# Kernel tuning notes

Hardware: AMD Instinct MI355X
Metric: run time of the kernel (lower is better)

## Reference

```python
import jax, jax.numpy as jnp
import numpy as np

SEQ, BATCH, EMBED = 1024, 2, 768
E = 16            # num_experts = m * N = 2 * 8
FFN_H = 1536      # expert_dim = ceil(3072 / 2)
K_SHARED = 1
K_ROUTE = 3       # (m * top_k) - k_shared = 4 - 1
LN_EPS = 1e-5
NEG_INF = -1e9


def setup_inputs() -> dict:
    key = jax.random.key(0)
    ks = jax.random.split(key, 4)
    x = jax.random.normal(ks[0], (SEQ, BATCH, EMBED), dtype=jnp.float32)
    gate_w = jax.random.normal(ks[1], (EMBED, E), dtype=jnp.float32) * 0.02
    gate_b = jnp.zeros((E,), jnp.float32)
    fc1_w = jax.random.normal(ks[2], (E, EMBED, FFN_H), dtype=jnp.float32) * 0.02
    fc1_b = jnp.zeros((E, FFN_H), jnp.float32)
    ln_w = jnp.ones((E, FFN_H), jnp.float32)
    ln_b = jnp.zeros((E, FFN_H), jnp.float32)
    fc2_w = jax.random.normal(ks[3], (E, FFN_H, EMBED), dtype=jnp.float32) * 0.02
    fc2_b = jnp.zeros((E, EMBED), jnp.float32)
    return {"x": x, "gate_w": gate_w, "gate_b": gate_b,
            "fc1_w": fc1_w, "fc1_b": fc1_b, "ln_w": ln_w, "ln_b": ln_b,
            "fc2_w": fc2_w, "fc2_b": fc2_b}


def reference(x, gate_w, gate_b, fc1_w, fc1_b, ln_w, ln_b, fc2_w, fc2_b):
    S, B, D = x.shape
    T = S * B
    xf = x.reshape(T, D)

    # --- gating: mask shared-expert logits, softmax, top-k over routed probs ---
    scores = xf @ gate_w + gate_b                      # [T, E]
    scores = scores.at[:, :K_SHARED].set(NEG_INF)
    probs = jax.nn.softmax(scores, axis=-1)
    topv, topi = jax.lax.top_k(probs, K_ROUTE)         # [T, K_ROUTE]

    # combine weights: gate prob for selected routed experts, 1.0 for shared experts
    combine = jnp.zeros((T, E), xf.dtype)
    combine = combine.at[jnp.arange(T)[:, None], topi].add(topv)
    combine = combine.at[:, :K_SHARED].add(1.0)        # shared expert(s), weight 1

    # --- per-expert FFN (dense over experts; combine zeros out unselected) ---
    h = jnp.einsum('td,edh->eth', xf, fc1_w) + fc1_b[:, None, :]   # [E, T, H]
    h = jax.nn.gelu(h, approximate=False)              # torch nn.GELU = exact erf
    mu = h.mean(-1, keepdims=True)
    var = h.var(-1, keepdims=True)
    h = (h - mu) * jax.lax.rsqrt(var + LN_EPS) * ln_w[:, None, :] + ln_b[:, None, :]
    y = jnp.einsum('eth,ehd->etd', h, fc2_w) + fc2_b[:, None, :]   # [E, T, D]

    # --- scatter-add combine (gate-weighted sum over experts) ---
    out = jnp.einsum('te,etd->td', combine, y)
    return out.reshape(S, B, D)
```

## Files before the change

kernel.cpp:

```cpp
#include <hip/hip_runtime.h>
#include <cmath>

#define T_TOK 2048
#define D_EMB 768
#define H_FFN 1536
#define NE    16
#define NPAIR (T_TOK * 4)

typedef __attribute__((ext_vector_type(8))) short          short8;
typedef __attribute__((ext_vector_type(8))) unsigned short ushort8;
typedef __attribute__((ext_vector_type(4))) unsigned short ushort4v;
typedef __attribute__((ext_vector_type(4))) float          floatx4;

__device__ __forceinline__ float bf2f(unsigned short u) {
  union { unsigned int i; float f; } v; v.i = ((unsigned int)u) << 16; return v.f;
}
__device__ __forceinline__ unsigned short f2bf(float f) {
  union { float f; unsigned int i; } v; v.f = f;
  unsigned int r = v.i + 0x7fffu + ((v.i >> 16) & 1u);
  return (unsigned short)(r >> 16);
}

__device__ __forceinline__ void gload16(const unsigned short* g, unsigned short* l) {
  __builtin_amdgcn_global_load_lds(
      (const __attribute__((address_space(1))) unsigned int*)g,
      (__attribute__((address_space(3))) unsigned int*)l,
      16, 0, 0);
}

__global__ __launch_bounds__(64) void sniff_kernel(
    const unsigned int* __restrict__ x, int* __restrict__ flag)
{
  int lane = threadIdx.x;
  int c = 0;
  for (int i = 0; i < 8; i++) {
    unsigned int w = x[i * 64 + lane];
    unsigned int e = (w >> 7) & 0xFFu;
    c += (e >= 100u && e <= 140u) ? 1 : 0;
  }
  for (int off = 32; off > 0; off >>= 1) c += __shfl_down(c, off);
  if (lane == 0) *flag = (c > 300) ? 1 : 0;
}

__global__ __launch_bounds__(256) void conv_kernel(
    const float* __restrict__ x, const float* __restrict__ fc1b,
    const float* __restrict__ lnw, const float* __restrict__ lnb,
    const float* __restrict__ fc2b,
    unsigned short* __restrict__ dx, unsigned short* __restrict__ dfc1b,
    unsigned short* __restrict__ dlnw, unsigned short* __restrict__ dlnb,
    unsigned short* __restrict__ dfc2b, const int* __restrict__ flag)
{
  if (*flag) return;
  int g = blockIdx.x * 256 + threadIdx.x;
#pragma unroll
  for (int i = 0; i < 3; i++) dx[g + i * 524288] = f2bf(x[g + i * 524288]);
  if (g < 24576) { dfc1b[g] = f2bf(fc1b[g]); dlnw[g] = f2bf(lnw[g]); dlnb[g] = f2bf(lnb[g]); }
  if (g < 12288) dfc2b[g] = f2bf(fc2b[g]);
}

template<int R, int C>
__global__ __launch_bounds__(256) void transpose_kernel(
    const unsigned short* __restrict__ srcB, const float* __restrict__ srcF,
    const int* __restrict__ flag, unsigned short* __restrict__ dst)
{
  __shared__ __align__(16) unsigned short tile[64][72];
  constexpr int RT = R / 64, CT = C / 64;
  int bx  = blockIdx.x;
  int e   = bx / (RT * CT);
  int rem = bx % (RT * CT);
  int rt  = rem / CT, ct = rem % CT;
  int tid = threadIdx.x;
  int r   = tid >> 2;
  int c   = (tid & 3) * 16;
  int xr  = (r & 7) * 8;
  size_t sbase = ((size_t)e * R + rt * 64 + r) * C + ct * 64 + c;
  if (*flag) {
    ushort8 v0 = *(const ushort8*)(srcB + sbase);
    ushort8 v1 = *(const ushort8*)(srcB + sbase + 8);
    *(ushort8*)&tile[r][(c) ^ xr]     = v0;
    *(ushort8*)&tile[r][(c + 8) ^ xr] = v1;
  } else {
    unsigned short tmp[16];
#pragma unroll
    for (int q = 0; q < 4; q++) {
      floatx4 f = *(const floatx4*)(srcF + sbase + q * 4);
#pragma unroll
      for (int j = 0; j < 4; j++) tmp[q * 4 + j] = f2bf(f[j]);
    }
    *(ushort8*)&tile[r][(c) ^ xr]     = *(ushort8*)&tmp[0];
    *(ushort8*)&tile[r][(c + 8) ^ xr] = *(ushort8*)&tmp[8];
  }
  __syncthreads();
  int n  = tid >> 2;
  int k  = (tid & 3) * 16;
  unsigned short outv[16];
#pragma unroll
  for (int j = 0; j < 16; j++) {
    int kr = k + j;
    outv[j] = tile[kr][n ^ ((kr & 7) * 8)];
  }
  size_t dbase = ((size_t)e * C + ct * 64 + n) * R + rt * 64 + k;
  *(ushort8*)(dst + dbase)     = *(ushort8*)&outv[0];
  *(ushort8*)(dst + dbase + 8) = *(ushort8*)&outv[8];
}

__global__ __launch_bounds__(64) void gate_kernel(
    const unsigned short* __restrict__ x16, const float* __restrict__ x32,
    const unsigned short* __restrict__ gw16, const float* __restrict__ gw32,
    const unsigned short* __restrict__ gb16, const float* __restrict__ gb32,
    const int* __restrict__ flag,
    int* __restrict__ psel, float* __restrict__ pw)
{
  int t = blockIdx.x;
  int lane = threadIdx.x;
  int isbf = *flag;
  float acc[NE];
#pragma unroll
  for (int e = 0; e < NE; e++) acc[e] = 0.f;
  if (isbf) {
#pragma unroll
    for (int i = 0; i < D_EMB / 64; i++) {
      int d = i * 64 + lane;
      float xv = bf2f(x16[(size_t)t * D_EMB + d]);
      ushort8 g0 = *(const ushort8*)(gw16 + d * NE);
      ushort8 g1 = *(const ushort8*)(gw16 + d * NE + 8);
#pragma unroll
      for (int e = 0; e < 8; e++) acc[e]     += xv * bf2f(g0[e]);
#pragma unroll
      for (int e = 0; e < 8; e++) acc[8 + e] += xv * bf2f(g1[e]);
    }
  } else {
#pragma unroll
    for (int i = 0; i < D_EMB / 64; i++) {
      int d = i * 64 + lane;
      float xv = x32[(size_t)t * D_EMB + d];
#pragma unroll
      for (int q = 0; q < 4; q++) {
        floatx4 g = *(const floatx4*)(gw32 + d * NE + q * 4);
#pragma unroll
        for (int j = 0; j < 4; j++) acc[q * 4 + j] += xv * g[j];
      }
    }
  }
  __shared__ __align__(16) float sacc[64][NE + 1];
#pragma unroll
  for (int e = 0; e < NE; e++) sacc[lane][e] = acc[e];
  __syncthreads();
  int e = lane & 15, q = lane >> 4;
  float s = 0.f;
#pragma unroll
  for (int i = 0; i < 16; i++) s += sacc[q * 16 + i][e];
  s += __shfl_xor(s, 16);
  s += __shfl_xor(s, 32);
  float sv = s + (isbf ? bf2f(gb16[e]) : gb32[e]);
  if (e == 0) sv = -1e9f;
  float m = sv;
#pragma unroll
  for (int off = 8; off > 0; off >>= 1) m = fmaxf(m, __shfl_xor(m, off));
  float pe = expf(sv - m);
  float den = pe;
#pragma unroll
  for (int off = 8; off > 0; off >>= 1) den += __shfl_xor(den, off);
  float pr = pe / den;
  float val = (e == 0) ? -1.f : pr;
  int sel0, sel1, sel2; float sw0, sw1, sw2;
#pragma unroll
  for (int k = 0; k < 3; k++) {
    float bv = val; int bi = e;
#pragma unroll
    for (int off = 8; off > 0; off >>= 1) {
      float ov = __shfl_xor(bv, off);
      int   oi = __shfl_xor(bi, off);
      if (ov > bv || (ov == bv && oi < bi)) { bv = ov; bi = oi; }
    }
    if (k == 0) { sel0 = bi; sw0 = bv; }
    else if (k == 1) { sel1 = bi; sw1 = bv; }
    else { sel2 = bi; sw2 = bv; }
    if (e == bi) val = -1.f;
  }
  if (lane == 0) {
    psel[t * 4] = 0;    pw[t * 4] = 1.0f;
    psel[t * 4 + 1] = sel0; pw[t * 4 + 1] = sw0;
    psel[t * 4 + 2] = sel1; pw[t * 4 + 2] = sw1;
    psel[t * 4 + 3] = sel2; pw[t * 4 + 3] = sw2;
  }
}

__global__ __launch_bounds__(256) void bucket_kernel(
    const int* __restrict__ psel, int* __restrict__ cnt, int* __restrict__ plist)
{
  int e = blockIdx.x;
  int tid = threadIdx.x;
  int wave = tid >> 6, lane = tid & 63;
  __shared__ int wsum[4];
  __shared__ int base;
  if (tid == 0) base = 0;
  __syncthreads();
  for (int c0 = 0; c0 < NPAIR; c0 += 256) {
    bool mt = (psel[c0 + tid] == e);
    unsigned long long mask = __ballot(mt);
    int wcount = __popcll(mask);
    if (lane == 0) wsum[wave] = wcount;
    __syncthreads();
    int wpre = 0;
#pragma unroll
    for (int w = 0; w < 4; w++) if (w < wave) wpre += wsum[w];
    int total = wsum[0] + wsum[1] + wsum[2] + wsum[3];
    if (mt) {
      int off = __popcll(mask & ((1ULL << lane) - 1ULL));
      plist[e * T_TOK + base + wpre + off] = c0 + tid;
    }
    __syncthreads();
    if (tid == 0) base += total;
    __syncthreads();
  }
  if (tid == 0) cnt[e] = base;
}

template<int KDIM, int NDIM, bool GELU, bool HASBIAS, bool AROWDIV4, bool OUTF32>
__global__ __launch_bounds__(256) void moe_gemm(
    const unsigned short* __restrict__ AO, const unsigned short* __restrict__ AC,
    const unsigned short* __restrict__ BT,
    const unsigned short* __restrict__ biasO, const unsigned short* __restrict__ biasC,
    const int* __restrict__ flag,
    const int* __restrict__ cnt, const int* __restrict__ plist,
    unsigned short* __restrict__ outB, float* __restrict__ outF)
{
  const int NSP = NDIM / 128;
  int bx  = blockIdx.x;
  int e   = bx / (16 * NSP);
  int rem = bx % (16 * NSP);
  int mt  = rem / NSP;
  int ns  = rem % NSP;
  int count = cnt[e];
  if (mt * 128 >= count) return;
  const unsigned short* Abase   = (*flag) ? AO : AC;
  const unsigned short* biasAll = (*flag) ? biasO : biasC;

  __shared__ __align__(16) unsigned short sA[128 * 64];
  __shared__ __align__(16) unsigned short sB[128 * 64];
  __shared__ int sp[128];

  int tid = threadIdx.x;
  if (tid < 128) {
    int rg  = mt * 128 + tid;
    int idx = rg < count ? rg : count - 1;
    sp[tid] = plist[e * T_TOK + idx];
  }
  __syncthreads();

  int lane = tid & 63;
  int wave = tid >> 6;
  int n0   = ns * 128;

  int lrow  = lane >> 3;
  int lsch  = (lane & 7) ^ lrow;
  const unsigned short* ag[4];
  const unsigned short* bg[4];
  unsigned short* la[4];
  unsigned short* lb[4];
#pragma unroll
  for (int s = 0; s < 4; s++) {
    int r  = wave * 32 + s * 8;
    int p  = sp[r + lrow];
    ag[s] = Abase + (size_t)(AROWDIV4 ? (p >> 2) : p) * KDIM + lsch * 8;
    bg[s] = BT + ((size_t)e * NDIM + n0 + r + lrow) * KDIM + lsch * 8;
    la[s] = sA + r * 64;
    lb[s] = sB + r * 64;
  }

  int m16  = lane & 15;
  int quad = lane >> 4;
  int wm   = (wave >> 1) * 64;
  int wn   = (wave & 1) * 64;
  int rsw  = (m16 & 7);

  floatx4 acc[4][4];
#pragma unroll
  for (int i = 0; i < 4; i++)
#pragma unroll
    for (int j = 0; j < 4; j++) acc[i][j] = (floatx4){0.f, 0.f, 0.f, 0.f};

  for (int k0 = 0; k0 < KDIM; k0 += 64) {
    if (k0) __syncthreads();
#pragma unroll
    for (int s = 0; s < 4; s++) gload16(ag[s] + k0, la[s]);
#pragma unroll
    for (int s = 0; s < 4; s++) gload16(bg[s] + k0, lb[s]);
    __syncthreads();
#pragma unroll
    for (int ks = 0; ks < 2; ks++) {
      int ch = ((ks * 4 + quad) ^ rsw) * 8;
      short8 af[4], bf[4];
#pragma unroll
      for (int m = 0; m < 4; m++)
        af[m] = *(const short8*)(sA + (wm + m * 16 + m16) * 64 + ch);
#pragma unroll
      for (int n = 0; n < 4; n++)
        bf[n] = *(const short8*)(sB + (wn + n * 16 + m16) * 64 + ch);
#pragma unroll
      for (int m = 0; m < 4; m++)
#pragma unroll
        for (int n = 0; n < 4; n++)
          acc[m][n] = __builtin_amdgcn_mfma_f32_16x16x32_bf16(af[m], bf[n], acc[m][n], 0, 0, 0);
    }
  }

#pragma unroll
  for (int m = 0; m < 4; m++) {
#pragma unroll
    for (int r = 0; r < 4; r++) {
      int row_local = wm + m * 16 + quad * 4 + r;
      int rg = mt * 128 + row_local;
      if (rg < count) {
        int p = sp[row_local];
#pragma unroll
        for (int n = 0; n < 4; n++) {
          int col = n0 + wn + n * 16 + m16;
          float v = acc[m][n][r];
          if (HASBIAS) v += bf2f(biasAll[e * NDIM + col]);
          if (GELU)    v = 0.5f * v * (1.f + erff(v * 0.70710678118654752f));
          if (OUTF32) outF[(size_t)p * NDIM + col] = v;
          else        outB[(size_t)p * NDIM + col] = f2bf(v);
        }
      }
    }
  }
}

__global__ __launch_bounds__(256) void ln_kernel(
    unsigned short* __restrict__ Hbuf,
    const unsigned short* __restrict__ lnwO, const unsigned short* __restrict__ lnwC,
    const unsigned short* __restrict__ lnbO, const unsigned short* __restrict__ lnbC,
    const int* __restrict__ psel, const float* __restrict__ pw,
    const int* __restrict__ flag)
{
  int p = blockIdx.x;
  int tid = threadIdx.x;
  int e = psel[p];
  int isbf = *flag;
  const unsigned short* lnw = isbf ? lnwO : lnwC;
  const unsigned short* lnb = isbf ? lnbO : lnbC;
  unsigned short* hr = Hbuf + (size_t)p * H_FFN;
  bool act = tid < 192;
  float v[8];
  float s = 0.f, sq = 0.f;
  if (act) {
    ushort8 hv = *(const ushort8*)(hr + tid * 8);
#pragma unroll
    for (int j = 0; j < 8; j++) { v[j] = bf2f(hv[j]); s += v[j]; sq += v[j] * v[j]; }
  }
#pragma unroll
  for (int off = 32; off > 0; off >>= 1) {
    s  += __shfl_down(s, off);
    sq += __shfl_down(sq, off);
  }
  __shared__ float red[8];
  int wave = tid >> 6, lane = tid & 63;
  if (lane == 0) { red[wave * 2] = s; red[wave * 2 + 1] = sq; }
  __syncthreads();
  __shared__ float mv[2];
  if (tid == 0) {
    float S = 0.f, Q = 0.f;
    for (int w = 0; w < 4; w++) { S += red[w * 2]; Q += red[w * 2 + 1]; }
    float mu  = S * (1.f / H_FFN);
    float var = Q * (1.f / H_FFN) - mu * mu;
    mv[0] = mu; mv[1] = rsqrtf(var + 1e-5f);
  }
  __syncthreads();
  if (act) {
    float mu = mv[0], rstd = mv[1];
    float w = pw[p];
    ushort8 lw = *(const ushort8*)(lnw + e * H_FFN + tid * 8);
    ushort8 lb = *(const ushort8*)(lnb + e * H_FFN + tid * 8);
    ushort8 o;
#pragma unroll
    for (int j = 0; j < 8; j++)
      o[j] = f2bf(((v[j] - mu) * rstd * bf2f(lw[j]) + bf2f(lb[j])) * w);
    *(ushort8*)(hr + tid * 8) = o;
  }
}

__global__ __launch_bounds__(256) void combine_kernel(
    const float* __restrict__ Y,
    const unsigned short* __restrict__ b2O, const unsigned short* __restrict__ b2C,
    const int* __restrict__ psel, const float* __restrict__ pw,
    unsigned short* __restrict__ out16, float* __restrict__ out32,
    const int* __restrict__ flag)
{
  int t = blockIdx.x;
  int tid = threadIdx.x;
  if (tid >= 192) return;
  int isbf = *flag;
  const unsigned short* b2 = isbf ? b2O : b2C;
  int e1 = psel[t * 4 + 1], e2 = psel[t * 4 + 2], e3 = psel[t * 4 + 3];
  float w1 = pw[t * 4 + 1], w2 = pw[t * 4 + 2], w3 = pw[t * 4 + 3];
  int d = tid * 4;
  const float* Yb = Y + (size_t)t * 4 * D_EMB + d;
  floatx4 y0 = *(const floatx4*)(Yb);
  floatx4 y1 = *(const floatx4*)(Yb + D_EMB);
  floatx4 y2 = *(const floatx4*)(Yb + 2 * D_EMB);
  floatx4 y3 = *(const floatx4*)(Yb + 3 * D_EMB);
  ushort4v b0 = *(const ushort4v*)(b2 + d);
  ushort4v bb1 = *(const ushort4v*)(b2 + e1 * D_EMB + d);
  ushort4v bb2 = *(const ushort4v*)(b2 + e2 * D_EMB + d);
  ushort4v bb3 = *(const ushort4v*)(b2 + e3 * D_EMB + d);
  if (isbf) {
    ushort4v o;
#pragma unroll
    for (int j = 0; j < 4; j++) {
      float a = y0[j] + y1[j] + y2[j] + y3[j] + bf2f(b0[j])
              + w1 * bf2f(bb1[j]) + w2 * bf2f(bb2[j]) + w3 * bf2f(bb3[j]);
      o[j] = f2bf(a);
    }
    *(ushort4v*)(out16 + (size_t)t * D_EMB + d) = o;
  } else {
    floatx4 o;
#pragma unroll
    for (int j = 0; j < 4; j++)
      o[j] = y0[j] + y1[j] + y2[j] + y3[j] + bf2f(b0[j])
           + w1 * bf2f(bb1[j]) + w2 * bf2f(bb2[j]) + w3 * bf2f(bb3[j]);
    *(floatx4*)(out32 + (size_t)t * D_EMB + d) = o;
  }
}

extern "C" void kernel_launch(void* const* d_in, const int* in_sizes, int n_in,
                              void* d_out, int out_size, void* d_ws, size_t ws_size,
                              hipStream_t stream)
{
  (void)in_sizes; (void)n_in; (void)out_size; (void)ws_size;
  char* ws = (char*)d_ws;
  int*   cnt   = (int*)ws;
  int*   plist = (int*)(ws + 256);
  int*   psel  = (int*)(ws + 131328);
  float* pw    = (float*)(ws + 164096);
  int*   flag  = (int*)(ws + 196864);
  unsigned short* fc1bC = (unsigned short*)(ws + 197120);
  unsigned short* lnwC  = (unsigned short*)(ws + 246272);
  unsigned short* lnbC  = (unsigned short*)(ws + 295424);
  unsigned short* fc2bC = (unsigned short*)(ws + 344576);
  unsigned short* xC    = (unsigned short*)(ws + 524288);
  unsigned short* Hbuf  = (unsigned short*)(ws + 3670016);
  float*          Ybuf  = (float*)(ws + 28835840);
  unsigned short* fc1T  = (unsigned short*)(ws + 54001664);
  unsigned short* fc2T  = (unsigned short*)(ws + 91750400);

  sniff_kernel<<<1, 64, 0, stream>>>((const unsigned int*)d_in[0], flag);

  conv_kernel<<<2048, 256, 0, stream>>>(
      (const float*)d_in[0], (const float*)d_in[4], (const float*)d_in[5],
      (const float*)d_in[6], (const float*)d_in[8],
      xC, fc1bC, lnwC, lnbC, fc2bC, flag);

  transpose_kernel<768, 1536><<<16 * 12 * 24, 256, 0, stream>>>(
      (const unsigned short*)d_in[3], (const float*)d_in[3], flag, fc1T);
  transpose_kernel<1536, 768><<<16 * 24 * 12, 256, 0, stream>>>(
      (const unsigned short*)d_in[7], (const float*)d_in[7], flag, fc2T);

  gate_kernel<<<T_TOK, 64, 0, stream>>>(
      (const unsigned short*)d_in[0], (const float*)d_in[0],
      (const unsigned short*)d_in[1], (const float*)d_in[1],
      (const unsigned short*)d_in[2], (const float*)d_in[2],
      flag, psel, pw);

  bucket_kernel<<<NE, 256, 0, stream>>>(psel, cnt, plist);

  moe_gemm<D_EMB, H_FFN, true, true, true, false>
      <<<NE * 16 * (H_FFN / 128), 256, 0, stream>>>(
      (const unsigned short*)d_in[0], xC, fc1T,
      (const unsigned short*)d_in[4], fc1bC,
      flag, cnt, plist, Hbuf, nullptr);

  ln_kernel<<<NPAIR, 256, 0, stream>>>(
      Hbuf,
      (const unsigned short*)d_in[5], lnwC,
      (const unsigned short*)d_in[6], lnbC,
      psel, pw, flag);

  moe_gemm<H_FFN, D_EMB, false, false, false, true>
      <<<NE * 16 * (D_EMB / 128), 256, 0, stream>>>(
      Hbuf, Hbuf, fc2T,
      nullptr, nullptr,
      flag, cnt, plist, nullptr, Ybuf);

  combine_kernel<<<T_TOK, 256, 0, stream>>>(
      Ybuf,
      (const unsigned short*)d_in[8], fc2bC,
      psel, pw,
      (unsigned short*)d_out, (float*)d_out, flag);
}
```

Baseline: 356.6 us.

## Fuse sniff, convert, transpose, gate and bucket into one prep kernel

Merges the dtype-sniff, fp32→bf16 conversion, both weight transposes, gating and expert bucketing into a single launch partitioned by block index. Each block repeats the sniff itself, and bucketing now uses atomicAdd on counters zeroed by a memset instead of a separate ordered scan. This removes several kernel launches and serialization points, and lets the transposes overlap with gating. In exchange, plist order is nondeterministic and every block pays a small sniff plus a barrier. The combine kernel also shrinks to 192 threads so no threads are idle.

```diff
diff --git a/kernel.cpp b/kernel.cpp
--- a/kernel.cpp
+++ b/kernel.cpp
@@ -7,6 +7,11 @@
 #define NE    16
 #define NPAIR (T_TOK * 4)
 
+#define NT1   4608
+#define NT2   4608
+#define NCONV 2048
+#define NGATE 512
+
 typedef __attribute__((ext_vector_type(8))) short          short8;
 typedef __attribute__((ext_vector_type(8))) unsigned short ushort8;
 typedef __attribute__((ext_vector_type(4))) unsigned short ushort4v;
@@ -28,53 +33,39 @@
       16, 0, 0);
 }
 
-__global__ __launch_bounds__(64) void sniff_kernel(
-    const unsigned int* __restrict__ x, int* __restrict__ flag)
-{
-  int lane = threadIdx.x;
+__device__ __forceinline__ int block_sniff(const unsigned int* __restrict__ xw, int tid) {
   int c = 0;
-  for (int i = 0; i < 8; i++) {
-    unsigned int w = x[i * 64 + lane];
+#pragma unroll
+  for (int i = 0; i < 2; i++) {
+    unsigned int w = xw[tid * 2 + i];
     unsigned int e = (w >> 7) & 0xFFu;
     c += (e >= 100u && e <= 140u) ? 1 : 0;
   }
+#pragma unroll
   for (int off = 32; off > 0; off >>= 1) c += __shfl_down(c, off);
-  if (lane == 0) *flag = (c > 300) ? 1 : 0;
-}
-
-__global__ __launch_bounds__(256) void conv_kernel(
-    const float* __restrict__ x, const float* __restrict__ fc1b,
-    const float* __restrict__ lnw, const float* __restrict__ lnb,
-    const float* __restrict__ fc2b,
-    unsigned short* __restrict__ dx, unsigned short* __restrict__ dfc1b,
-    unsigned short* __restrict__ dlnw, unsigned short* __restrict__ dlnb,
-    unsigned short* __restrict__ dfc2b, const int* __restrict__ flag)
-{
-  if (*flag) return;
-  int g = blockIdx.x * 256 + threadIdx.x;
-#pragma unroll
-  for (int i = 0; i < 3; i++) dx[g + i * 524288] = f2bf(x[g + i * 524288]);
-  if (g < 24576) { dfc1b[g] = f2bf(fc1b[g]); dlnw[g] = f2bf(lnw[g]); dlnb[g] = f2bf(lnb[g]); }
-  if (g < 12288) dfc2b[g] = f2bf(fc2b[g]);
+  __shared__ int ssn[4];
+  int wave = tid >> 6, lane = tid & 63;
+  if (lane == 0) ssn[wave] = c;
+  __syncthreads();
+  return (ssn[0] + ssn[1] + ssn[2] + ssn[3] > 300) ? 1 : 0;
 }
 
 template<int R, int C>
-__global__ __launch_bounds__(256) void transpose_kernel(
+__device__ __forceinline__ void transpose_body(
     const unsigned short* __restrict__ srcB, const float* __restrict__ srcF,
-    const int* __restrict__ flag, unsigned short* __restrict__ dst)
-{
-  __shared__ __align__(16) unsigned short tile[64][72];
+    int isbf, unsigned short* __restrict__ dst, int bx, int tid,
+    unsigned char* smemraw)
+{
+  auto tile = (unsigned short(*)[72])smemraw;
   constexpr int RT = R / 64, CT = C / 64;
-  int bx  = blockIdx.x;
   int e   = bx / (RT * CT);
   int rem = bx % (RT * CT);
   int rt  = rem / CT, ct = rem % CT;
-  int tid = threadIdx.x;
   int r   = tid >> 2;
   int c   = (tid & 3) * 16;
   int xr  = (r & 7) * 8;
   size_t sbase = ((size_t)e * R + rt * 64 + r) * C + ct * 64 + c;
-  if (*flag) {
+  if (isbf) {
     ushort8 v0 = *(const ushort8*)(srcB + sbase);
     ushort8 v1 = *(const ushort8*)(srcB + sbase + 8);
     *(ushort8*)&tile[r][(c) ^ xr]     = v0;
@@ -104,117 +95,120 @@
   *(ushort8*)(dst + dbase + 8) = *(ushort8*)&outv[8];
 }
 
-__global__ __launch_bounds__(64) void gate_kernel(
+__global__ __launch_bounds__(256) void prep_kernel(
+    const unsigned int* __restrict__ xw,
     const unsigned short* __restrict__ x16, const float* __restrict__ x32,
     const unsigned short* __restrict__ gw16, const float* __restrict__ gw32,
     const unsigned short* __restrict__ gb16, const float* __restrict__ gb32,
-    const int* __restrict__ flag,
-    int* __restrict__ psel, float* __restrict__ pw)
-{
-  int t = blockIdx.x;
-  int lane = threadIdx.x;
-  int isbf = *flag;
-  float acc[NE];
-#pragma unroll
-  for (int e = 0; e < NE; e++) acc[e] = 0.f;
-  if (isbf) {
-#pragma unroll
-    for (int i = 0; i < D_EMB / 64; i++) {
-      int d = i * 64 + lane;
-      float xv = bf2f(x16[(size_t)t * D_EMB + d]);
-      ushort8 g0 = *(const ushort8*)(gw16 + d * NE);
-      ushort8 g1 = *(const ushort8*)(gw16 + d * NE + 8);
-#pragma unroll
-      for (int e = 0; e < 8; e++) acc[e]     += xv * bf2f(g0[e]);
-#pragma unroll
-      for (int e = 0; e < 8; e++) acc[8 + e] += xv * bf2f(g1[e]);
+    const unsigned short* __restrict__ w1B, const float* __restrict__ w1F,
+    const unsigned short* __restrict__ w2B, const float* __restrict__ w2F,
+    const float* __restrict__ fc1bF, const float* __restrict__ lnwF,
+    const float* __restrict__ lnbF, const float* __restrict__ fc2bF,
+    unsigned short* __restrict__ xC,
+    unsigned short* __restrict__ dfc1b, unsigned short* __restrict__ dlnw,
+    unsigned short* __restrict__ dlnb, unsigned short* __restrict__ dfc2b,
+    unsigned short* __restrict__ fc1T, unsigned short* __restrict__ fc2T,
+    int* __restrict__ flagOut,
+    int* __restrict__ psel, float* __restrict__ pw,
+    int* __restrict__ cnt, int* __restrict__ plist)
+{
+  __shared__ __align__(16) unsigned char smem[4 * 64 * 17 * 4];
+  int bid = blockIdx.x;
+  int tid = threadIdx.x;
+  int isbf = block_sniff(xw, tid);
+  if (bid == 0 && tid == 0) *flagOut = isbf;
+
+  if (bid < NT1) {
+    transpose_body<768, 1536>(w1B, w1F, isbf, fc1T, bid, tid, smem);
+  } else if (bid < NT1 + NT2) {
+    transpose_body<1536, 768>(w2B, w2F, isbf, fc2T, bid - NT1, tid, smem);
+  } else if (bid < NT1 + NT2 + NCONV) {
+    if (!isbf) {
+      int g = (bid - NT1 - NT2) * 256 + tid;
+#pragma unroll
+      for (int i = 0; i < 3; i++) xC[g + i * 524288] = f2bf(x32[g + i * 524288]);
+      if (g < 24576) { dfc1b[g] = f2bf(fc1bF[g]); dlnw[g] = f2bf(lnwF[g]); dlnb[g] = f2bf(lnbF[g]); }
+      if (g < 12288) dfc2b[g] = f2bf(fc2bF[g]);
     }
   } else {
-#pragma unroll
-    for (int i = 0; i < D_EMB / 64; i++) {
-      int d = i * 64 + lane;
-      float xv = x32[(size_t)t * D_EMB + d];
-#pragma unroll
-      for (int q = 0; q < 4; q++) {
-        floatx4 g = *(const floatx4*)(gw32 + d * NE + q * 4);
-#pragma unroll
-        for (int j = 0; j < 4; j++) acc[q * 4 + j] += xv * g[j];
+    int wave = tid >> 6, lane = tid & 63;
+    int t = (bid - (NT1 + NT2 + NCONV)) * 4 + wave;
+    float acc[NE];
+#pragma unroll
+    for (int e = 0; e < NE; e++) acc[e] = 0.f;
+    if (isbf) {
+#pragma unroll
+      for (int i = 0; i < D_EMB / 64; i++) {
+        int d = i * 64 + lane;
+        float xv = bf2f(x16[(size_t)t * D_EMB + d]);
+        ushort8 g0 = *(const ushort8*)(gw16 + d * NE);
+        ushort8 g1 = *(const ushort8*)(gw16 + d * NE + 8);
+#pragma unroll
+        for (int e = 0; e < 8; e++) acc[e]     += xv * bf2f(g0[e]);
+#pragma unroll
+        for (int e = 0; e < 8; e++) acc[8 + e] += xv * bf2f(g1[e]);
       }
-    }
-  }
-  __shared__ __align__(16) float sacc[64][NE + 1];
-#pragma unroll
-  for (int e = 0; e < NE; e++) sacc[lane][e] = acc[e];
-  __syncthreads();
-  int e = lane & 15, q = lane >> 4;
-  float s = 0.f;
-#pragma unroll
-  for (int i = 0; i < 16; i++) s += sacc[q * 16 + i][e];
-  s += __shfl_xor(s, 16);
-  s += __shfl_xor(s, 32);
-  float sv = s + (isbf ? bf2f(gb16[e]) : gb32[e]);
-  if (e == 0) sv = -1e9f;
-  float m = sv;
-#pragma unroll
-  for (int off = 8; off > 0; off >>= 1) m = fmaxf(m, __shfl_xor(m, off));
-  float pe = expf(sv - m);
-  float den = pe;
-#pragma unroll
-  for (int off = 8; off > 0; off >>= 1) den += __shfl_xor(den, off);
-  float pr = pe / den;
-  float val = (e == 0) ? -1.f : pr;
-  int sel0, sel1, sel2; float sw0, sw1, sw2;
-#pragma unroll
-  for (int k = 0; k < 3; k++) {
-    float bv = val; int bi = e;
-#pragma unroll
-    for (int off = 8; off > 0; off >>= 1) {
-      float ov = __shfl_xor(bv, off);
-      int   oi = __shfl_xor(bi, off);
-      if (ov > bv || (ov == bv && oi < bi)) { bv = ov; bi = oi; }
-    }
-    if (k == 0) { sel0 = bi; sw0 = bv; }
-    else if (k == 1) { sel1 = bi; sw1 = bv; }
-    else { sel2 = bi; sw2 = bv; }
-    if (e == bi) val = -1.f;
-  }
-  if (lane == 0) {
-    psel[t * 4] = 0;    pw[t * 4] = 1.0f;
-    psel[t * 4 + 1] = sel0; pw[t * 4 + 1] = sw0;
-    psel[t * 4 + 2] = sel1; pw[t * 4 + 2] = sw1;
-    psel[t * 4 + 3] = sel2; pw[t * 4 + 3] = sw2;
-  }
-}
-
-__global__ __launch_bounds__(256) void bucket_kernel(
-    const int* __restrict__ psel, int* __restrict__ cnt, int* __restrict__ plist)
-{
-  int e = blockIdx.x;
-  int tid = threadIdx.x;
-  int wave = tid >> 6, lane = tid & 63;
-  __shared__ int wsum[4];
-  __shared__ int base;
-  if (tid == 0) base = 0;
-  __syncthreads();
-  for (int c0 = 0; c0 < NPAIR; c0 += 256) {
-    bool mt = (psel[c0 + tid] == e);
-    unsigned long long mask = __ballot(mt);
-    int wcount = __popcll(mask);
-    if (lane == 0) wsum[wave] = wcount;
+    } else {
+#pragma unroll
+      for (int i = 0; i < D_EMB / 64; i++) {
+        int d = i * 64 + lane;
+        float xv = x32[(size_t)t * D_EMB + d];
+#pragma unroll
+        for (int q = 0; q < 4; q++) {
+          floatx4 g = *(const floatx4*)(gw32 + d * NE + q * 4);
+#pragma unroll
+          for (int j = 0; j < 4; j++) acc[q * 4 + j] += xv * g[j];
+        }
+      }
+    }
+    auto sacc = (float(*)[64][17])smem;
+#pragma unroll
+    for (int e = 0; e < NE; e++) sacc[wave][lane][e] = acc[e];
     __syncthreads();
-    int wpre = 0;
-#pragma unroll
-    for (int w = 0; w < 4; w++) if (w < wave) wpre += wsum[w];
-    int total = wsum[0] + wsum[1] + wsum[2] + wsum[3];
-    if (mt) {
-      int off = __popcll(mask & ((1ULL << lane) - 1ULL));
-      plist[e * T_TOK + base + wpre + off] = c0 + tid;
-    }
-    __syncthreads();
-    if (tid == 0) base += total;
-    __syncthreads();
-  }
-  if (tid == 0) cnt[e] = base;
+    int e = lane & 15, q = lane >> 4;
+    float s = 0.f;
+#pragma unroll
+    for (int i = 0; i < 16; i++) s += sacc[wave][q * 16 + i][e];
+    s += __shfl_xor(s, 16);
+    s += __shfl_xor(s, 32);
+    float sv = s + (isbf ? bf2f(gb16[e]) : gb32[e]);
+    if (e == 0) sv = -1e9f;
+    float m = sv;
+#pragma unroll
+    for (int off = 8; off > 0; off >>= 1) m = fmaxf(m, __shfl_xor(m, off));
+    float pe = expf(sv - m);
+    float den = pe;
+#pragma unroll
+    for (int off = 8; off > 0; off >>= 1) den += __shfl_xor(den, off);
+    float pr = pe / den;
+    float val = (e == 0) ? -1.f : pr;
+    int sel0, sel1, sel2; float sw0, sw1, sw2;
+#pragma unroll
+    for (int k = 0; k < 3; k++) {
+      float bv = val; int bi = e;
+#pragma unroll
+      for (int off = 8; off > 0; off >>= 1) {
+        float ov = __shfl_xor(bv, off);
+        int   oi = __shfl_xor(bi, off);
+        if (ov > bv || (ov == bv && oi < bi)) { bv = ov; bi = oi; }
+      }
+      if (k == 0) { sel0 = bi; sw0 = bv; }
+      else if (k == 1) { sel1 = bi; sw1 = bv; }
+      else { sel2 = bi; sw2 = bv; }
+      if (e == bi) val = -1.f;
+    }
+    if (lane < 4) {
+      int se; float swt;
+      if (lane == 0)      { se = 0;    swt = 1.0f; }
+      else if (lane == 1) { se = sel0; swt = sw0; }
+      else if (lane == 2) { se = sel1; swt = sw1; }
+      else                { se = sel2; swt = sw2; }
+      int pidx = t * 4 + lane;
+      psel[pidx] = se; pw[pidx] = swt;
+      int pos = atomicAdd(&cnt[se], 1);
+      plist[se * T_TOK + pos] = pidx;
+    }
+  }
 }
 
 template<int KDIM, int NDIM, bool GELU, bool HASBIAS, bool AROWDIV4, bool OUTF32>
@@ -257,16 +251,14 @@
   int lsch  = (lane & 7) ^ lrow;
   const unsigned short* ag[4];
   const unsigned short* bg[4];
-  unsigned short* la[4];
-  unsigned short* lb[4];
+  int loff[4];
 #pragma unroll
   for (int s = 0; s < 4; s++) {
     int r  = wave * 32 + s * 8;
     int p  = sp[r + lrow];
     ag[s] = Abase + (size_t)(AROWDIV4 ? (p >> 2) : p) * KDIM + lsch * 8;
     bg[s] = BT + ((size_t)e * NDIM + n0 + r + lrow) * KDIM + lsch * 8;
-    la[s] = sA + r * 64;
-    lb[s] = sB + r * 64;
+    loff[s] = r * 64;
   }
 
   int m16  = lane & 15;
@@ -284,9 +276,9 @@
   for (int k0 = 0; k0 < KDIM; k0 += 64) {
     if (k0) __syncthreads();
 #pragma unroll
-    for (int s = 0; s < 4; s++) gload16(ag[s] + k0, la[s]);
-#pragma unroll
-    for (int s = 0; s < 4; s++) gload16(bg[s] + k0, lb[s]);
+    for (int s = 0; s < 4; s++) gload16(ag[s] + k0, sA + loff[s]);
+#pragma unroll
+    for (int s = 0; s < 4; s++) gload16(bg[s] + k0, sB + loff[s]);
     __syncthreads();
 #pragma unroll
     for (int ks = 0; ks < 2; ks++) {
@@ -381,7 +373,7 @@
   }
 }
 
-__global__ __launch_bounds__(256) void combine_kernel(
+__global__ __launch_bounds__(192) void combine_kernel(
     const float* __restrict__ Y,
     const unsigned short* __restrict__ b2O, const unsigned short* __restrict__ b2C,
     const int* __restrict__ psel, const float* __restrict__ pw,
@@ -390,7 +382,6 @@
 {
   int t = blockIdx.x;
   int tid = threadIdx.x;
-  if (tid >= 192) return;
   int isbf = *flag;
   const unsigned short* b2 = isbf ? b2O : b2C;
   int e1 = psel[t * 4 + 1], e2 = psel[t * 4 + 2], e3 = psel[t * 4 + 3];
@@ -445,25 +436,20 @@
   unsigned short* fc1T  = (unsigned short*)(ws + 54001664);
   unsigned short* fc2T  = (unsigned short*)(ws + 91750400);
 
-  sniff_kernel<<<1, 64, 0, stream>>>((const unsigned int*)d_in[0], flag);
-
-  conv_kernel<<<2048, 256, 0, stream>>>(
-      (const float*)d_in[0], (const float*)d_in[4], (const float*)d_in[5],
-      (const float*)d_in[6], (const float*)d_in[8],
-      xC, fc1bC, lnwC, lnbC, fc2bC, flag);
-
-  transpose_kernel<768, 1536><<<16 * 12 * 24, 256, 0, stream>>>(
-      (const unsigned short*)d_in[3], (const float*)d_in[3], flag, fc1T);
-  transpose_kernel<1536, 768><<<16 * 24 * 12, 256, 0, stream>>>(
-      (const unsigned short*)d_in[7], (const float*)d_in[7], flag, fc2T);
-
-  gate_kernel<<<T_TOK, 64, 0, stream>>>(
+  hipMemsetAsync(cnt, 0, 64, stream);
+
+  prep_kernel<<<NT1 + NT2 + NCONV + NGATE, 256, 0, stream>>>(
+      (const unsigned int*)d_in[0],
       (const unsigned short*)d_in[0], (const float*)d_in[0],
       (const unsigned short*)d_in[1], (const float*)d_in[1],
       (const unsigned short*)d_in[2], (const float*)d_in[2],
-      flag, psel, pw);
-
-  bucket_kernel<<<NE, 256, 0, stream>>>(psel, cnt, plist);
+      (const unsigned short*)d_in[3], (const float*)d_in[3],
+      (const unsigned short*)d_in[7], (const float*)d_in[7],
+      (const float*)d_in[4], (const float*)d_in[5],
+      (const float*)d_in[6], (const float*)d_in[8],
+      xC, fc1bC, lnwC, lnbC, fc2bC,
+      fc1T, fc2T,
+      flag, psel, pw, cnt, plist);
 
   moe_gemm<D_EMB, H_FFN, true, true, true, false>
       <<<NE * 16 * (H_FFN / 128), 256, 0, stream>>>(
@@ -483,7 +469,7 @@
       nullptr, nullptr,
       flag, cnt, plist, nullptr, Ybuf);
 
-  combine_kernel<<<T_TOK, 256, 0, stream>>>(
+  combine_kernel<<<T_TOK, 192, 0, stream>>>(
       Ybuf,
       (const unsigned short*)d_in[8], fc2bC,
       psel, pw,
```

After: 354.2 us. Within noise of the previous version (-0.7%).
